# Optimization experiments

Hardware: AMD Instinct MI355X
Metric: run time of the kernel (lower is better)

Reference implementation:

```python
import jax, jax.numpy as jnp
import numpy as np

D_MODEL = 1024
N_DIM = 64      # per-head dim; scores scaled by 1/sqrt(n_dim)
N_HEADS = 16
SEQ = 4096
LN_EPS = 1e-5


def setup_inputs() -> dict:
    key = jax.random.key(0)
    ks = jax.random.split(key, 12)
    hd = N_HEADS * N_DIM  # == D_MODEL (required by residual add)
    s = 0.02
    return {
        "embed_word_vec": jax.random.normal(ks[0], (SEQ, D_MODEL), dtype=jnp.float32),
        "attn_mask": jax.random.uniform(ks[1], (SEQ, SEQ)) < 0.1,  # True = masked out
        "wq": jax.random.normal(ks[2], (D_MODEL, hd), dtype=jnp.float32) * s,
        "bq": jnp.zeros((hd,), dtype=jnp.float32),
        "wk": jax.random.normal(ks[3], (D_MODEL, hd), dtype=jnp.float32) * s,
        "bk": jnp.zeros((hd,), dtype=jnp.float32),
        "wv": jax.random.normal(ks[4], (D_MODEL, hd), dtype=jnp.float32) * s,
        "bv": jnp.zeros((hd,), dtype=jnp.float32),
        "wo": jax.random.normal(ks[5], (hd, D_MODEL), dtype=jnp.float32) * s,
        "bo": jnp.zeros((D_MODEL,), dtype=jnp.float32),
        "gamma": jnp.ones((D_MODEL,), dtype=jnp.float32),
        "beta": jnp.zeros((D_MODEL,), dtype=jnp.float32),
    }


def reference(embed_word_vec, attn_mask, wq, bq, wk, bk, wv, bv, wo, bo, gamma, beta):
    x = embed_word_vec                      # [S, d_model]
    q = x @ wq + bq                         # [S, H*D]
    k = x @ wk + bk
    v = x @ wv + bv
    scores = (q @ k.T) / jnp.sqrt(jnp.asarray(N_DIM, dtype=q.dtype))  # [S, S]
    scores = jnp.where(attn_mask, jnp.asarray(-jnp.inf, dtype=scores.dtype), scores)
    attention = jax.nn.softmax(scores, axis=-1)                       # [S, S]
    context = attention @ v + x             # AV + residual, [S, d_model]
    h = context @ wo + bo                   # out projection
    # LayerNorm over last dim
    mu = jnp.mean(h, axis=-1, keepdims=True)
    var = jnp.mean(jnp.square(h - mu), axis=-1, keepdims=True)
    output = (h - mu) * jax.lax.rsqrt(var + LN_EPS) * gamma + beta
    return (output, attention)
```

## Files before the change

### kernel.cpp

```cpp
#include <hip/hip_runtime.h>
#include <hip/hip_bf16.h>
#include <stdint.h>

#define SEQ 4096
#define DM  1024

typedef __attribute__((ext_vector_type(8))) short bf16x8;
typedef __attribute__((ext_vector_type(4))) float f32x4;

template <int V> struct Int { static constexpr int v = V; };

__device__ __forceinline__ short f2bf(float f) {
  union { float f; unsigned int i; } x; x.f = f;
  unsigned int r = x.i + 0x7FFFu + ((x.i >> 16) & 1u);
  return (short)(r >> 16);
}
__device__ __forceinline__ float bf2f(short s) {
  union { unsigned int i; float f; } u;
  u.i = ((unsigned int)(unsigned short)s) << 16;
  return u.f;
}

__device__ __forceinline__ void gload16(const short* g, short* l) {
  __builtin_amdgcn_global_load_lds(
      (const __attribute__((address_space(1))) unsigned int*)g,
      (__attribute__((address_space(3))) unsigned int*)l, 16, 0, 0);
}

__device__ __forceinline__ float wave_max(float v) {
#pragma unroll
  for (int o = 32; o; o >>= 1) v = fmaxf(v, __shfl_xor(v, o));
  return v;
}
__device__ __forceinline__ float wave_sum(float v) {
#pragma unroll
  for (int o = 32; o; o >>= 1) v += __shfl_xor(v, o);
  return v;
}

#define BARRIER() do { asm volatile("" ::: "memory"); \
  __builtin_amdgcn_s_barrier(); asm volatile("" ::: "memory"); } while (0)
#define MF(a, b, c) __builtin_amdgcn_mfma_f32_16x16x32_bf16(a, b, c, 0, 0, 0)

template <int EPI>
__global__ __launch_bounds__(512, 2) void gemm8(
    const short* __restrict__ A, const short* __restrict__ B,
    short* __restrict__ C, const float* __restrict__ bias,
    int Ksplit, int lda, int ldb, int ldc,
    float scale, int ntm, int ntn, long csplit) {
  __shared__ short lds[2][4][8192];
  const int tid = threadIdx.x;
  const int lane = tid & 63;
  const int wid = tid >> 6;
  const int wr = wid >> 2;
  const int wc = wid & 3;
  const int bid = blockIdx.x, nwg = gridDim.x;
  int wg = (bid & 7) * (nwg >> 3) + (bid >> 3);
  const int tpg = ntm * ntn;
  const int split = wg / tpg;
  wg -= split * tpg;
  const int m0 = (wg / ntn) * 256;
  const int n0 = (wg % ntn) * 256;
  const short* Ab = A + (long)split * Ksplit;
  const short* Bb = B + (long)split * Ksplit;
  short* Co = C + (long)split * csplit;

  const int o0 = tid * 16;
  const int oo = o0 ^ (((o0 >> 7) & 7) << 4);
  const int sr0 = oo >> 7;
  const int sc0 = (oo & 127) >> 1;

  auto stA = [&](int buf, int h, int kt) {
    const short* g = Ab + (long)(m0 + h * 128 + sr0) * lda + kt * 64 + sc0;
    short* l = &lds[buf][h][0] + wid * 512;
    gload16(g, l);
    gload16(g + (long)64 * lda, l + 4096);
  };
  auto stB = [&](int buf, int h, int kt) {
    const short* g = Bb + (long)(n0 + h * 128 + sr0) * ldb + kt * 64 + sc0;
    short* l = &lds[buf][2 + h][0] + wid * 512;
    gload16(g, l);
    gload16(g + (long)64 * ldb, l + 4096);
  };

  const int ll = lane & 15, lh = lane >> 4;
  auto ldaf = [&](int buf, int c, int mm, int kk) {
    const int r = c * 32 + mm * 16 + ll;
    const int off = (r * 64 + kk * 32 + lh * 8) ^ ((r & 7) << 3);
    return *(const bf16x8*)(&lds[buf][wr][0] + off);
  };
  auto ldbf = [&](int buf, int n, int kk) {
    const int r = (wc & 1) * 64 + n * 16 + ll;
    const int off = (r * 64 + kk * 32 + lh * 8) ^ ((r & 7) << 3);
    return *(const bf16x8*)(&lds[buf][2 + (wc >> 1)][0] + off);
  };

  f32x4 acc[8][4];
#pragma unroll
  for (int i = 0; i < 8; i++)
#pragma unroll
    for (int j = 0; j < 4; j++) acc[i][j] = (f32x4){0.f, 0.f, 0.f, 0.f};
  bf16x8 Bf[4][2];

  const int NT = Ksplit >> 6;
  stB(0, 0, 0); stB(0, 1, 0);
  stA(0, 0, 0); stA(0, 1, 0);
  stB(1, 0, 1); stB(1, 1, 1);
  asm volatile("s_waitcnt vmcnt(4)" ::: "memory");
  BARRIER();

  auto phase = [&](auto BUF, auto CC, auto LB, auto&& stg, auto&& tail) {
    constexpr int buf = decltype(BUF)::v;
    constexpr int c = decltype(CC)::v;
    if constexpr (decltype(LB)::v != 0) {
#pragma unroll
      for (int n = 0; n < 4; n++) {
        Bf[n][0] = ldbf(buf, n, 0);
        Bf[n][1] = ldbf(buf, n, 1);
      }
    }
    bf16x8 a00 = ldaf(buf, c, 0, 0), a01 = ldaf(buf, c, 0, 1);
    bf16x8 a10 = ldaf(buf, c, 1, 0), a11 = ldaf(buf, c, 1, 1);
    stg();
    BARRIER();
    __builtin_amdgcn_s_setprio(1);
#pragma unroll
    for (int n = 0; n < 4; n++) {
      acc[2 * c][n] = MF(a00, Bf[n][0], acc[2 * c][n]);
      acc[2 * c][n] = MF(a01, Bf[n][1], acc[2 * c][n]);
      acc[2 * c + 1][n] = MF(a10, Bf[n][0], acc[2 * c + 1][n]);
      acc[2 * c + 1][n] = MF(a11, Bf[n][1], acc[2 * c + 1][n]);
    }
    __builtin_amdgcn_s_setprio(0);
    tail();
    BARRIER();
  };

  for (int t = 0; t < NT; t += 2) {
    const bool nl = (t + 2 < NT);
    phase(Int<0>{}, Int<0>{}, Int<1>{},
          [&] { stA(1, 0, t + 1); stA(1, 1, t + 1); }, [] {});
    phase(Int<0>{}, Int<1>{}, Int<0>{},
          [&] { if (nl) { stB(0, 0, t + 2); stB(0, 1, t + 2); } }, [] {});
    phase(Int<0>{}, Int<2>{}, Int<0>{}, [] {}, [] {});
    phase(Int<0>{}, Int<3>{}, Int<0>{}, [] {}, [&] {
      if (nl) { asm volatile("s_waitcnt vmcnt(4)" ::: "memory"); }
      else    { asm volatile("s_waitcnt vmcnt(0)" ::: "memory"); }
    });
    phase(Int<1>{}, Int<0>{}, Int<1>{},
          [&] { if (nl) { stA(0, 0, t + 2); stA(0, 1, t + 2); } }, [] {});
    phase(Int<1>{}, Int<1>{}, Int<0>{},
          [&] { if (nl) { stB(1, 0, t + 3); stB(1, 1, t + 3); } }, [] {});
    phase(Int<1>{}, Int<2>{}, Int<0>{}, [] {}, [] {});
    phase(Int<1>{}, Int<3>{}, Int<0>{}, [] {}, [&] {
      if (nl) { asm volatile("s_waitcnt vmcnt(4)" ::: "memory"); }
      else    { asm volatile("s_waitcnt vmcnt(0)" ::: "memory"); }
    });
  }

  const int rb = m0 + wr * 128 + lh * 4;
  const int cb0 = n0 + wc * 64 + ll;
#pragma unroll
  for (int mi = 0; mi < 8; mi++) {
#pragma unroll
    for (int n = 0; n < 4; n++) {
      const int col = cb0 + n * 16;
      float bv = 0.f;
      if (EPI == 1) bv = bias[col];
#pragma unroll
      for (int r = 0; r < 4; r++) {
        const int row = rb + mi * 16 + r;
        const long off = (long)row * ldc + col;
        float v = acc[mi][n][r];
        if (EPI == 1) v += bv;
        if (EPI == 2) v *= scale;
        Co[off] = f2bf(v);
      }
    }
  }
}


__global__ __launch_bounds__(256) void cvt_f32_to_bf16(
    const float* __restrict__ in, short* __restrict__ out, int n4) {
  int i = blockIdx.x * 256 + threadIdx.x;
  if (i < n4) {
    float4 f = ((const float4*)in)[i];
    short4 o;
    o.x = f2bf(f.x); o.y = f2bf(f.y); o.z = f2bf(f.z); o.w = f2bf(f.w);
    ((short4*)out)[i] = o;
  }
}

__global__ void transpose_w4(const float* __restrict__ s0,
                             const float* __restrict__ s1,
                             const float* __restrict__ s2,
                             const float* __restrict__ s3,
                             short* __restrict__ d0, short* __restrict__ d1,
                             short* __restrict__ d2, short* __restrict__ d3) {
  const int z = blockIdx.z;
  const float* in = z == 0 ? s0 : z == 1 ? s1 : z == 2 ? s2 : s3;
  short* out = z == 0 ? d0 : z == 1 ? d1 : z == 2 ? d2 : d3;
  __shared__ float tile[32][33];
  const int bx = blockIdx.x * 32;
  const int by = blockIdx.y * 32;
  const int tx = threadIdx.x, ty = threadIdx.y;
#pragma unroll
  for (int i = 0; i < 32; i += 8)
    tile[ty + i][tx] = in[(long)(by + ty + i) * 1024 + bx + tx];
  __syncthreads();
#pragma unroll
  for (int i = 0; i < 32; i += 8)
    out[(long)(bx + ty + i) * 1024 + by + tx] = f2bf(tile[tx][ty + i]);
}

__global__ void transpose_b_ld(const short* __restrict__ in,
                               short* __restrict__ out, int R, int C, int ldin) {
  __shared__ short tile[32][33];
  const int bx = blockIdx.x * 32;
  const int by = blockIdx.y * 32;
  const int tx = threadIdx.x, ty = threadIdx.y;
#pragma unroll
  for (int i = 0; i < 32; i += 8)
    tile[ty + i][tx] = in[(long)(by + ty + i) * ldin + bx + tx];
  __syncthreads();
#pragma unroll
  for (int i = 0; i < 32; i += 8)
    out[(long)(bx + ty + i) * R + by + tx] = tile[tx][ty + i];
}

__global__ __launch_bounds__(256) void concat_bias(
    const float* __restrict__ bq, const float* __restrict__ bk,
    const float* __restrict__ bv, float* __restrict__ o) {
  int i = blockIdx.x * 256 + threadIdx.x;
  float v = (i < 1024) ? bq[i] : (i < 2048 ? bk[i - 1024] : bv[i - 2048]);
  o[i] = v;
}

__global__ __launch_bounds__(256) void softmax_rows(const short* __restrict__ Sb,
                                                    const int* __restrict__ mask,
                                                    short* __restrict__ Pb) {
  const long row = blockIdx.x;
  const bf16x8* src = (const bf16x8*)(Sb + row * SEQ);
  const int* mrow = mask + row * (long)SEQ;
  bf16x8* dst = (bf16x8*)(Pb + row * SEQ);
  const int tid = threadIdx.x;
  const int wid = tid >> 6, lane = tid & 63;
  bf16x8 a = src[tid], b = src[tid + 256];
  int4 ma0 = *(const int4*)(mrow + tid * 8);
  int4 ma1 = *(const int4*)(mrow + tid * 8 + 4);
  int4 mb0 = *(const int4*)(mrow + 2048 + tid * 8);
  int4 mb1 = *(const int4*)(mrow + 2048 + tid * 8 + 4);
  float v[16];
#pragma unroll
  for (int j = 0; j < 8; j++) { v[j] = bf2f(a[j]); v[8 + j] = bf2f(b[j]); }
  const int* mm0 = (const int*)&ma0;
  const int* mm1 = (const int*)&ma1;
  const int* mm2 = (const int*)&mb0;
  const int* mm3 = (const int*)&mb1;
#pragma unroll
  for (int j = 0; j < 4; j++) {
    if (mm0[j]) v[j] = -INFINITY;
    if (mm1[j]) v[4 + j] = -INFINITY;
    if (mm2[j]) v[8 + j] = -INFINITY;
    if (mm3[j]) v[12 + j] = -INFINITY;
  }
  float mx = -INFINITY;
#pragma unroll
  for (int j = 0; j < 16; j++) mx = fmaxf(mx, v[j]);
  mx = wave_max(mx);
  __shared__ float red[4];
  if (lane == 0) red[wid] = mx;
  __syncthreads();
  mx = fmaxf(fmaxf(red[0], red[1]), fmaxf(red[2], red[3]));
  float sum = 0.f;
#pragma unroll
  for (int j = 0; j < 16; j++) {
    v[j] = __expf(v[j] - mx);
    sum += v[j];
  }
  sum = wave_sum(sum);
  __shared__ float red2[4];
  if (lane == 0) red2[wid] = sum;
  __syncthreads();
  sum = red2[0] + red2[1] + red2[2] + red2[3];
  const float inv = 1.0f / sum;
  bf16x8 o0, o1;
#pragma unroll
  for (int j = 0; j < 8; j++) {
    o0[j] = f2bf(v[j] * inv);
    o1[j] = f2bf(v[8 + j] * inv);
  }
  dst[tid] = o0;
  dst[tid + 256] = o1;
}

__global__ __launch_bounds__(256) void expand_bf16_f32(
    const short* __restrict__ in, float* __restrict__ out) {
  long i = (long)blockIdx.x * 256 + threadIdx.x;
  bf16x8 a = ((const bf16x8*)in)[i];
  float4 lo, hi;
  lo.x = bf2f(a[0]); lo.y = bf2f(a[1]); lo.z = bf2f(a[2]); lo.w = bf2f(a[3]);
  hi.x = bf2f(a[4]); hi.y = bf2f(a[5]); hi.z = bf2f(a[6]); hi.w = bf2f(a[7]);
  ((float4*)out)[2 * i] = lo;
  ((float4*)out)[2 * i + 1] = hi;
}

__global__ __launch_bounds__(256) void reduce_ctx4(
    const short* __restrict__ p, const float* __restrict__ x,
    short* __restrict__ cb) {
  const long i = (long)blockIdx.x * 256 + threadIdx.x;
  bf16x8 a = ((const bf16x8*)p)[i];
  bf16x8 b = ((const bf16x8*)(p + 4194304))[i];
  bf16x8 c = ((const bf16x8*)(p + 8388608))[i];
  bf16x8 d = ((const bf16x8*)(p + 12582912))[i];
  float4 x0 = ((const float4*)x)[2 * i];
  float4 x1 = ((const float4*)x)[2 * i + 1];
  float xs[8] = {x0.x, x0.y, x0.z, x0.w, x1.x, x1.y, x1.z, x1.w};
  bf16x8 o;
#pragma unroll
  for (int j = 0; j < 8; j++)
    o[j] = f2bf(bf2f(a[j]) + bf2f(b[j]) + bf2f(c[j]) + bf2f(d[j]) + xs[j]);
  ((bf16x8*)cb)[i] = o;
}

__global__ __launch_bounds__(256) void ln4(
    const short* __restrict__ ph, const float* __restrict__ bo,
    const float* __restrict__ gamma, const float* __restrict__ beta,
    float* __restrict__ out) {
  const long row = blockIdx.x;
  const int tid = threadIdx.x;
  const int wid = tid >> 6, lane = tid & 63;
  const long base = row * DM + tid * 4;
  short4 p0 = *(const short4*)(ph + base);
  short4 p1 = *(const short4*)(ph + 4194304 + base);
  short4 p2 = *(const short4*)(ph + 8388608 + base);
  short4 p3 = *(const short4*)(ph + 12582912 + base);
  float4 bb = *(const float4*)(bo + tid * 4);
  float v[4];
  v[0] = bf2f(p0.x) + bf2f(p1.x) + bf2f(p2.x) + bf2f(p3.x) + bb.x;
  v[1] = bf2f(p0.y) + bf2f(p1.y) + bf2f(p2.y) + bf2f(p3.y) + bb.y;
  v[2] = bf2f(p0.z) + bf2f(p1.z) + bf2f(p2.z) + bf2f(p3.z) + bb.z;
  v[3] = bf2f(p0.w) + bf2f(p1.w) + bf2f(p2.w) + bf2f(p3.w) + bb.w;
  float s = v[0] + v[1] + v[2] + v[3];
  s = wave_sum(s);
  __shared__ float red[4];
  if (lane == 0) red[wid] = s;
  __syncthreads();
  const float mu = (red[0] + red[1] + red[2] + red[3]) * (1.f / DM);
  float var = 0.f;
#pragma unroll
  for (int j = 0; j < 4; j++) {
    float d = v[j] - mu;
    var += d * d;
  }
  var = wave_sum(var);
  __shared__ float red2[4];
  if (lane == 0) red2[wid] = var;
  __syncthreads();
  var = (red2[0] + red2[1] + red2[2] + red2[3]) * (1.f / DM);
  const float inv = rsqrtf(var + 1e-5f);
  float4 g = *(const float4*)(gamma + tid * 4);
  float4 be = *(const float4*)(beta + tid * 4);
  float4 o;
  o.x = (v[0] - mu) * inv * g.x + be.x;
  o.y = (v[1] - mu) * inv * g.y + be.y;
  o.z = (v[2] - mu) * inv * g.z + be.z;
  o.w = (v[3] - mu) * inv * g.w + be.w;
  *(float4*)(out + base) = o;
}

extern "C" void kernel_launch(void* const* d_in, const int* in_sizes, int n_in,
                              void* d_out, int out_size, void* d_ws,
                              size_t ws_size, hipStream_t stream) {
  const float* x    = (const float*)d_in[0];
  const int* mask   = (const int*)d_in[1];
  const float* wq   = (const float*)d_in[2];
  const float* bq   = (const float*)d_in[3];
  const float* wk   = (const float*)d_in[4];
  const float* bk   = (const float*)d_in[5];
  const float* wv   = (const float*)d_in[6];
  const float* bv   = (const float*)d_in[7];
  const float* wo   = (const float*)d_in[8];
  const float* bo   = (const float*)d_in[9];
  const float* gamma = (const float*)d_in[10];
  const float* beta  = (const float*)d_in[11];

  float* out  = (float*)d_out;
  float* attn = out + 4194304;
  short* Sb   = (short*)attn;
  short* pav  = (short*)attn;
  short* ph   = (short*)(attn + 8388608);
  short* cbuf = (short*)out;

  char* w = (char*)d_ws;
  short* wqkvT = (short*)(w + 0);
  short* woT   = (short*)(w + 6291456);
  short* xb    = (short*)(w + 8388608);
  short* qkv   = (short*)(w + 16777216);
  short* attnb = (short*)(w + 8388608);
  short* vT    = (short*)(w + 41943040);
  float* bqkv  = (float*)(w + 50331648);

  cvt_f32_to_bf16<<<4096, 256, 0, stream>>>(x, xb, 1048576);
  transpose_w4<<<dim3(32, 32, 4), dim3(32, 8), 0, stream>>>(
      wq, wk, wv, wo, wqkvT, wqkvT + 1048576, wqkvT + 2097152, woT);
  concat_bias<<<12, 256, 0, stream>>>(bq, bk, bv, bqkv);

  gemm8<1><<<192, 512, 0, stream>>>(xb, wqkvT, qkv, bqkv,
                                    1024, 1024, 1024, 3072, 1.f, 16, 12, 0);

  transpose_b_ld<<<dim3(32, 128), dim3(32, 8), 0, stream>>>(qkv + 2048, vT,
                                                            4096, 1024, 3072);

  gemm8<2><<<256, 512, 0, stream>>>(qkv, qkv + 1024, Sb, nullptr,
                                    1024, 3072, 3072, 4096, 0.125f, 16, 16, 0);

  softmax_rows<<<SEQ, 256, 0, stream>>>(Sb, mask, attnb);

  gemm8<0><<<256, 512, 0, stream>>>(attnb, vT, pav, nullptr,
                                    1024, 4096, 4096, 1024, 1.f, 16, 4,
                                    4194304L);

  reduce_ctx4<<<2048, 256, 0, stream>>>(pav, x, cbuf);

  gemm8<0><<<256, 512, 0, stream>>>(cbuf, woT, ph, nullptr,
                                    256, 1024, 1024, 1024, 1.f, 16, 4,
                                    4194304L);

  ln4<<<SEQ, 256, 0, stream>>>(ph, bo, gamma, beta, out);

  expand_bf16_f32<<<8192, 256, 0, stream>>>(attnb, attn);
}
```

Baseline: 206.9 us.

## Fuse V transpose into QKV GEMM epilogue, reduce barriers, patch tile swizzle

The QKV projection GEMM now writes the V columns straight into a transposed vT buffer in its epilogue, which removes the separate transpose kernel and its global round-trip. The GEMM main loop drops the trailing barrier in each phase and keeps one barrier per half-iteration, moving the B-tile stage to a later phase. Workgroup-to-tile mapping now uses a patch-based swizzle so that XCD-local groups share rows and columns for better L2 reuse. The transposed epilogue store is strided (short4 per column row) and may be less coalesced, and the barrier reduction raises the risk of LDS hazards if the staging order is wrong.

```diff
diff --git a/kernel.cpp b/kernel.cpp
--- a/kernel.cpp
+++ b/kernel.cpp
@@ -45,9 +45,9 @@
 template <int EPI>
 __global__ __launch_bounds__(512, 2) void gemm8(
     const short* __restrict__ A, const short* __restrict__ B,
-    short* __restrict__ C, const float* __restrict__ bias,
-    int Ksplit, int lda, int ldb, int ldc,
-    float scale, int ntm, int ntn, long csplit) {
+    short* __restrict__ C, short* __restrict__ Cv,
+    const float* __restrict__ bias, int Ksplit, int lda, int ldb, int ldc,
+    int ldv, float scale, int ntm, int ntn, long csplit, int pc) {
   __shared__ short lds[2][4][8192];
   const int tid = threadIdx.x;
   const int lane = tid & 63;
@@ -55,12 +55,15 @@
   const int wr = wid >> 2;
   const int wc = wid & 3;
   const int bid = blockIdx.x, nwg = gridDim.x;
-  int wg = (bid & 7) * (nwg >> 3) + (bid >> 3);
+  const int chunk = nwg >> 3;
+  const int wl = (bid & 7) * chunk + (bid >> 3);
   const int tpg = ntm * ntn;
-  const int split = wg / tpg;
-  wg -= split * tpg;
-  const int m0 = (wg / ntn) * 256;
-  const int n0 = (wg % ntn) * 256;
+  const int split = wl / tpg;
+  const int r0 = wl - split * tpg;
+  const int q = r0 / chunk, i0 = r0 % chunk;
+  const int npatch = ntn / pc;
+  const int m0 = ((q / npatch) * (chunk / pc) + i0 / pc) * 256;
+  const int n0 = ((q % npatch) * pc + i0 % pc) * 256;
   const short* Ab = A + (long)split * Ksplit;
   const short* Bb = B + (long)split * Ksplit;
   short* Co = C + (long)split * csplit;
@@ -109,7 +112,7 @@
   asm volatile("s_waitcnt vmcnt(4)" ::: "memory");
   BARRIER();
 
-  auto phase = [&](auto BUF, auto CC, auto LB, auto&& stg, auto&& tail) {
+  auto phase = [&](auto BUF, auto CC, auto LB, auto BARv, auto&& stg) {
     constexpr int buf = decltype(BUF)::v;
     constexpr int c = decltype(CC)::v;
     if constexpr (decltype(LB)::v != 0) {
@@ -122,7 +125,7 @@
     bf16x8 a00 = ldaf(buf, c, 0, 0), a01 = ldaf(buf, c, 0, 1);
     bf16x8 a10 = ldaf(buf, c, 1, 0), a11 = ldaf(buf, c, 1, 1);
     stg();
-    BARRIER();
+    if constexpr (decltype(BARv)::v != 0) BARRIER();
     __builtin_amdgcn_s_setprio(1);
 #pragma unroll
     for (int n = 0; n < 4; n++) {
@@ -132,47 +135,63 @@
       acc[2 * c + 1][n] = MF(a11, Bf[n][1], acc[2 * c + 1][n]);
     }
     __builtin_amdgcn_s_setprio(0);
-    tail();
-    BARRIER();
   };
 
   for (int t = 0; t < NT; t += 2) {
     const bool nl = (t + 2 < NT);
-    phase(Int<0>{}, Int<0>{}, Int<1>{},
-          [&] { stA(1, 0, t + 1); stA(1, 1, t + 1); }, [] {});
-    phase(Int<0>{}, Int<1>{}, Int<0>{},
-          [&] { if (nl) { stB(0, 0, t + 2); stB(0, 1, t + 2); } }, [] {});
-    phase(Int<0>{}, Int<2>{}, Int<0>{}, [] {}, [] {});
-    phase(Int<0>{}, Int<3>{}, Int<0>{}, [] {}, [&] {
-      if (nl) { asm volatile("s_waitcnt vmcnt(4)" ::: "memory"); }
-      else    { asm volatile("s_waitcnt vmcnt(0)" ::: "memory"); }
-    });
-    phase(Int<1>{}, Int<0>{}, Int<1>{},
-          [&] { if (nl) { stA(0, 0, t + 2); stA(0, 1, t + 2); } }, [] {});
-    phase(Int<1>{}, Int<1>{}, Int<0>{},
-          [&] { if (nl) { stB(1, 0, t + 3); stB(1, 1, t + 3); } }, [] {});
-    phase(Int<1>{}, Int<2>{}, Int<0>{}, [] {}, [] {});
-    phase(Int<1>{}, Int<3>{}, Int<0>{}, [] {}, [&] {
-      if (nl) { asm volatile("s_waitcnt vmcnt(4)" ::: "memory"); }
-      else    { asm volatile("s_waitcnt vmcnt(0)" ::: "memory"); }
-    });
+    phase(Int<0>{}, Int<0>{}, Int<1>{}, Int<0>{},
+          [&] { stA(1, 0, t + 1); stA(1, 1, t + 1); });
+    phase(Int<0>{}, Int<1>{}, Int<0>{}, Int<1>{}, [] {});
+    phase(Int<0>{}, Int<2>{}, Int<0>{}, Int<1>{},
+          [&] { if (nl) { stB(0, 0, t + 2); stB(0, 1, t + 2); } });
+    phase(Int<0>{}, Int<3>{}, Int<0>{}, Int<1>{}, [] {});
+    if (nl) { asm volatile("s_waitcnt vmcnt(4)" ::: "memory"); }
+    else    { asm volatile("s_waitcnt vmcnt(0)" ::: "memory"); }
+    BARRIER();
+    phase(Int<1>{}, Int<0>{}, Int<1>{}, Int<0>{},
+          [&] { if (nl) { stA(0, 0, t + 2); stA(0, 1, t + 2); } });
+    phase(Int<1>{}, Int<1>{}, Int<0>{}, Int<1>{}, [] {});
+    phase(Int<1>{}, Int<2>{}, Int<0>{}, Int<1>{},
+          [&] { if (nl) { stB(1, 0, t + 3); stB(1, 1, t + 3); } });
+    phase(Int<1>{}, Int<3>{}, Int<0>{}, Int<1>{}, [] {});
+    if (nl) {
+      asm volatile("s_waitcnt vmcnt(4)" ::: "memory");
+      BARRIER();
+    }
   }
 
   const int rb = m0 + wr * 128 + lh * 4;
   const int cb0 = n0 + wc * 64 + ll;
+  if (EPI == 3 && n0 >= 2048) {
+#pragma unroll
+    for (int mi = 0; mi < 8; mi++) {
+#pragma unroll
+      for (int n = 0; n < 4; n++) {
+        const int col = cb0 + n * 16;
+        const float bv = bias[col];
+        short4 pk;
+        pk.x = f2bf(acc[mi][n][0] + bv);
+        pk.y = f2bf(acc[mi][n][1] + bv);
+        pk.z = f2bf(acc[mi][n][2] + bv);
+        pk.w = f2bf(acc[mi][n][3] + bv);
+        *(short4*)(Cv + (long)(col - 2048) * ldv + rb + mi * 16) = pk;
+      }
+    }
+    return;
+  }
 #pragma unroll
   for (int mi = 0; mi < 8; mi++) {
 #pragma unroll
     for (int n = 0; n < 4; n++) {
       const int col = cb0 + n * 16;
       float bv = 0.f;
-      if (EPI == 1) bv = bias[col];
+      if (EPI == 1 || EPI == 3) bv = bias[col];
 #pragma unroll
       for (int r = 0; r < 4; r++) {
         const int row = rb + mi * 16 + r;
         const long off = (long)row * ldc + col;
         float v = acc[mi][n][r];
-        if (EPI == 1) v += bv;
+        if (EPI == 1 || EPI == 3) v += bv;
         if (EPI == 2) v *= scale;
         Co[off] = f2bf(v);
       }
@@ -212,21 +231,6 @@
 #pragma unroll
   for (int i = 0; i < 32; i += 8)
     out[(long)(bx + ty + i) * 1024 + by + tx] = f2bf(tile[tx][ty + i]);
-}
-
-__global__ void transpose_b_ld(const short* __restrict__ in,
-                               short* __restrict__ out, int R, int C, int ldin) {
-  __shared__ short tile[32][33];
-  const int bx = blockIdx.x * 32;
-  const int by = blockIdx.y * 32;
-  const int tx = threadIdx.x, ty = threadIdx.y;
-#pragma unroll
-  for (int i = 0; i < 32; i += 8)
-    tile[ty + i][tx] = in[(long)(by + ty + i) * ldin + bx + tx];
-  __syncthreads();
-#pragma unroll
-  for (int i = 0; i < 32; i += 8)
-    out[(long)(bx + ty + i) * R + by + tx] = tile[tx][ty + i];
 }
 
 __global__ __launch_bounds__(256) void concat_bias(
@@ -407,26 +411,25 @@
       wq, wk, wv, wo, wqkvT, wqkvT + 1048576, wqkvT + 2097152, woT);
   concat_bias<<<12, 256, 0, stream>>>(bq, bk, bv, bqkv);
 
-  gemm8<1><<<192, 512, 0, stream>>>(xb, wqkvT, qkv, bqkv,
-                                    1024, 1024, 1024, 3072, 1.f, 16, 12, 0);
-
-  transpose_b_ld<<<dim3(32, 128), dim3(32, 8), 0, stream>>>(qkv + 2048, vT,
-                                                            4096, 1024, 3072);
-
-  gemm8<2><<<256, 512, 0, stream>>>(qkv, qkv + 1024, Sb, nullptr,
-                                    1024, 3072, 3072, 4096, 0.125f, 16, 16, 0);
+  gemm8<3><<<192, 512, 0, stream>>>(xb, wqkvT, qkv, vT, bqkv,
+                                    1024, 1024, 1024, 3072, 4096, 1.f,
+                                    16, 12, 0, 6);
+
+  gemm8<2><<<256, 512, 0, stream>>>(qkv, qkv + 1024, Sb, nullptr, nullptr,
+                                    1024, 3072, 3072, 4096, 0, 0.125f,
+                                    16, 16, 0, 8);
 
   softmax_rows<<<SEQ, 256, 0, stream>>>(Sb, mask, attnb);
 
-  gemm8<0><<<256, 512, 0, stream>>>(attnb, vT, pav, nullptr,
-                                    1024, 4096, 4096, 1024, 1.f, 16, 4,
-                                    4194304L);
+  gemm8<0><<<256, 512, 0, stream>>>(attnb, vT, pav, nullptr, nullptr,
+                                    1024, 4096, 4096, 1024, 0, 1.f,
+                                    16, 4, 4194304L, 4);
 
   reduce_ctx4<<<2048, 256, 0, stream>>>(pav, x, cbuf);
 
-  gemm8<0><<<256, 512, 0, stream>>>(cbuf, woT, ph, nullptr,
-                                    256, 1024, 1024, 1024, 1.f, 16, 4,
-                                    4194304L);
+  gemm8<0><<<256, 512, 0, stream>>>(cbuf, woT, ph, nullptr, nullptr,
+                                    256, 1024, 1024, 1024, 0, 1.f,
+                                    16, 4, 4194304L, 4);
 
   ln4<<<SEQ, 256, 0, stream>>>(ph, bo, gamma, beta, out);
 
```

Result: faster. 196.8 us (-4.9%).
